# Kernel optimization log

Hardware: AMD Instinct MI355X
Metric: run time of the kernel (lower is better)

Reference implementation:

```python
import jax, jax.numpy as jnp
import numpy as np
from jax import lax

# Lens/aperture geometry (must match init_kwargs lens_mask)
LENS = 21
RADIUS = LENS // 2
EPS = 1e-8


def _offsets():
    """Flattened 21x21 aperture footprint: distance kernel, circular lens mask,
    and (row, col) slice offsets into the padded image."""
    ys, xs = np.meshgrid(np.arange(LENS), np.arange(LENS), indexing='ij')
    dy = ys - RADIUS
    dx = xs - RADIUS
    dist = np.sqrt(dy * dy + dx * dx).astype(np.float32)
    mask = (dist <= RADIUS).astype(np.float32)
    return (jnp.asarray(dist.ravel()), jnp.asarray(mask.ravel()),
            jnp.asarray(ys.ravel().astype(np.int32)),
            jnp.asarray(xs.ravel().astype(np.int32)))


def scatter_layer(x5, lens_effect):
    """Scatter (splat) defocus rendering of one RGBAD layer.

    x5: [B,5,H,W] (r,g,b,alpha,relative-disparity); lens_effect: [B,1].
    Each source pixel splats its premultiplied color over a disk of radius
    r = |disp| * lens_effect (soft-edged, area-normalized). Because the disk
    kernel is symmetric in the offset, the scatter is computed as a gather
    over the 21x21 footprint with weights taken from the *source* pixel.

    Returns [B,5,H,W]: [:3] accumulated rgb, [3] accumulated weight,
    [4] occupancy (clipped accumulated alpha-weight).
    """
    B, _, H, W = x5.shape
    dist, mask, oy, ox = _offsets()
    rgb, a, disp = x5[:, :3], x5[:, 3:4], x5[:, 4:5]
    r = jnp.clip(jnp.abs(disp) * lens_effect[:, :, None, None], 0.0, float(RADIUS))  # [B,1,H,W]

    # per-source-pixel soft disk area: sum_o mask(o) * clip(r + 0.5 - dist(o), 0, 1)
    def area_step(acc, dm):
        d, m = dm
        return acc + m * jnp.clip(r + 0.5 - d, 0.0, 1.0), None

    area, _ = lax.scan(area_step, jnp.zeros_like(r), (dist, mask))

    # premultiplied source energy, normalized by splat area
    s = jnp.concatenate([rgb * a, a], axis=1) / (area + EPS)  # [B,4,H,W]
    pad = ((0, 0), (0, 0), (RADIUS, RADIUS), (RADIUS, RADIUS))
    s_pad = jnp.pad(s, pad)
    r_pad = jnp.pad(r, pad)

    # gather formulation of the scatter: out[q] = sum_o s[q-o] * w(o; r[q-o])
    def step(acc, dmyx):
        d, m, dy, dx = dmyx
        sl = lax.dynamic_slice(s_pad, (0, 0, dy, dx), (B, 4, H, W))
        rsl = lax.dynamic_slice(r_pad, (0, 0, dy, dx), (B, 1, H, W))
        w = m * jnp.clip(rsl + 0.5 - d, 0.0, 1.0)
        return acc + sl * w, None

    out4, _ = lax.scan(step, jnp.zeros((B, 4, H, W), x5.dtype), (dist, mask, oy, ox))
    occu = jnp.clip(out4[:, 3:4], 0.0, 1.0)
    return jnp.concatenate([out4, occu], axis=1)


def setup_inputs() -> dict:
    key = jax.random.key(0)
    k1, k2 = jax.random.split(key)
    B, N_LAYER, H, W = 2, 3, 512, 512
    rgbad_layers = jax.random.uniform(k1, (B, 5 * N_LAYER, H, W), dtype=jnp.float32)
    # lens strength in a range that exercises the full 21x21 footprint
    lens_effect = jax.random.uniform(k2, (B, 1), dtype=jnp.float32) * 10.0
    focal = jnp.zeros((B, 5 * N_LAYER, H, W), dtype=jnp.float32)
    return {"rgbad_layers": rgbad_layers, "lens_effect": lens_effect, "focal": focal}


def reference(rgbad_layers, lens_effect, focal):
    """Multi_Layer_Renderer.forward: front-to-back alpha compositing of
    per-layer scatter-rendered bokeh."""
    x = rgbad_layers - focal
    n_layer = x.shape[1] // 5
    blurs = [scatter_layer(x[:, 5 * i:5 * (i + 1)], lens_effect) for i in range(n_layer)]
    rgb0, w0, o0 = blurs[0][:, :3], blurs[0][:, 3:4], blurs[0][:, 4:5]
    blur_rgb = rgb0 / (w0 + EPS) * o0
    trans = 1.0 - o0  # accumulated transmittance
    for li in range(1, n_layer):
        lr, lw, lo = blurs[li][:, :3], blurs[li][:, 3:4], blurs[li][:, 4:5]
        blur_rgb = blur_rgb + lr / (lw + EPS) * (trans * lo)
        trans = trans * (1.0 - lo)
    return blur_rgb
```

## Files before the change

### kernel.cpp

```cpp
#include <hip/hip_runtime.h>
#include <hip/hip_bf16.h>

#define HH 512
#define WW 512
#define HWSZ (512*512)

typedef _Float16 hh4 __attribute__((ext_vector_type(4)));

__device__ __forceinline__ float clamp01(float x) {
    return __builtin_amdgcn_fmed3f(x, 0.0f, 1.0f);
}

__global__ __launch_bounds__(256, 2)
void mlr_kernel(const float* __restrict__ rgbad,
                const float* __restrict__ lens_eff,
                const float* __restrict__ focal,
                float* __restrict__ out)
{
    constexpr int TW = 64, TH = 16;
    constexpr int SW = TW + 20;
    constexpr int SH = TH + 20;
    constexpr int LP = SW + 1;

    __shared__ uint2 sL[SH * LP];
    __shared__ float rL[SH * LP];
    __shared__ int   maxbits;

    const int tx  = threadIdx.x;
    const int ty  = threadIdx.y;
    const int tid = ty * 16 + tx;
    const int bx0 = blockIdx.x * TW;
    const int by0 = blockIdx.y * TH;
    const int bb  = blockIdx.z;
    const float lens = lens_eff[bb];

    static constexpr float DJ[44] = {
        0.f, 1.f, 1.41421356f, 2.f, 2.23606798f, 2.82842712f, 3.f, 3.16227766f,
        3.60555128f, 4.f, 4.12310563f, 4.24264069f, 4.47213595f, 5.f, 5.09901951f,
        5.38516481f, 5.65685425f, 5.83095189f, 6.f, 6.08276253f, 6.32455532f,
        6.40312424f, 6.70820393f, 7.f, 7.07106781f, 7.21110255f, 7.28010989f,
        7.61577311f, 7.81024968f, 8.f, 8.06225775f, 8.24621125f, 8.48528137f,
        8.54400375f, 8.60232527f, 8.94427191f, 9.f, 9.05538514f, 9.21954446f,
        9.43398113f, 9.48683298f, 9.84885780f, 9.89949494f, 10.f };
    static constexpr float CNT[44] = {
        1,4,4,4,8,4,4,8,8,4,8,4,8,12,8,8,4,8,4,8,8,8,
        8,4,12,8,8,8,8,4,16,8,4,8,8,8,4,8,16,8,8,8,4,12 };

    float blurR[4] = {0,0,0,0}, blurG[4] = {0,0,0,0}, blurB[4] = {0,0,0,0};
    float trans[4] = {1,1,1,1};

#pragma unroll 1
    for (int l = 0; l < 3; ++l) {
        __syncthreads();
        if (tid == 0) maxbits = 0;
        __syncthreads();

        const float* pin = rgbad + (size_t)(bb * 15 + 5 * l) * HWSZ;
        const float* pfo = focal + (size_t)(bb * 15 + 5 * l) * HWSZ;
        float mloc = 0.f;
#pragma unroll 1
        for (int i = tid; i < SH * SW; i += 256) {
            const int row = i / SW;
            const int col = i - row * SW;
            const int gy = by0 - 10 + row;
            const int gx = bx0 - 10 + col;
            uint2 pk; pk.x = 0u; pk.y = 0u;
            float rp05 = 0.f;
            if ((unsigned)gy < (unsigned)HH && (unsigned)gx < (unsigned)WW) {
                const int off = gy * WW + gx;
                const float cr = pin[off]            - pfo[off];
                const float cg = pin[off +   HWSZ]   - pfo[off +   HWSZ];
                const float cb = pin[off + 2*HWSZ]   - pfo[off + 2*HWSZ];
                const float ca = pin[off + 3*HWSZ]   - pfo[off + 3*HWSZ];
                const float cd = pin[off + 4*HWSZ]   - pfo[off + 4*HWSZ];
                const float r  = fminf(fabsf(cd) * lens, 10.f);
                rp05 = r + 0.5f;
                float a0 = 0.f, a1 = 0.f;
#pragma unroll
                for (int j = 0; j < 44; j += 2) {
                    a0 = fmaf(CNT[j],     clamp01(rp05 - DJ[j]),     a0);
                    a1 = fmaf(CNT[j + 1], clamp01(rp05 - DJ[j + 1]), a1);
                }
                const float inv = 1.0f / (a0 + a1 + 1e-8f);
                const float pa  = ca * inv;
                hh4 hv;
                hv.x = (_Float16)(cr * pa);
                hv.y = (_Float16)(cg * pa);
                hv.z = (_Float16)(cb * pa);
                hv.w = (_Float16)pa;
                pk = __builtin_bit_cast(uint2, hv);
                mloc = fmaxf(mloc, rp05);
            }
            sL[row * LP + col] = pk;
            rL[row * LP + col] = rp05;
        }
        atomicMax(&maxbits, __float_as_int(mloc));
        __syncthreads();

        const float rmax = __int_as_float(maxbits);
        const int U = min(10, (int)ceilf(rmax) - 1);

        float accR[4] = {0,0,0,0}, accG[4] = {0,0,0,0};
        float accB[4] = {0,0,0,0}, accW[4] = {0,0,0,0};

#pragma unroll 1
        for (int u = -U; u <= U; ++u) {
            const float u2f = (float)(u * u);
            float dd[21];
#pragma unroll
            for (int k = 0; k < 21; ++k) {
                const int dxk = k - 10;
                const float q = u2f + (float)(dxk * dxk);
                dd[k] = (q <= 100.0f) ? __builtin_sqrtf(q) : 1e9f;
            }
            const int rbase = (ty + 10 + u) * LP + 10 + 4 * tx;
#pragma unroll
            for (int v = -10; v <= 13; ++v) {
                const float rp = rL[rbase + v];
                const uint2 sp = sL[rbase + v];
                const hh4 hv = __builtin_bit_cast(hh4, sp);
                const float s0 = (float)hv.x;
                const float s1 = (float)hv.y;
                const float s2 = (float)hv.z;
                const float s3 = (float)hv.w;
#pragma unroll
                for (int ox = 0; ox < 4; ++ox) {
                    const int dx = v - ox;
                    if (dx >= -10 && dx <= 10) {
                        const float w = clamp01(rp - dd[dx + 10]);
                        accR[ox] = fmaf(s0, w, accR[ox]);
                        accG[ox] = fmaf(s1, w, accG[ox]);
                        accB[ox] = fmaf(s2, w, accB[ox]);
                        accW[ox] = fmaf(s3, w, accW[ox]);
                    }
                }
            }
        }

#pragma unroll
        for (int ox = 0; ox < 4; ++ox) {
            const float wsum = accW[ox];
            const float occ  = clamp01(wsum);
            const float f    = trans[ox] * occ / (wsum + 1e-8f);
            blurR[ox] = fmaf(accR[ox], f, blurR[ox]);
            blurG[ox] = fmaf(accG[ox], f, blurG[ox]);
            blurB[ox] = fmaf(accB[ox], f, blurB[ox]);
            trans[ox] *= (1.0f - occ);
        }
    }

    const int oy = by0 + ty;
    const size_t obase = (size_t)bb * 3 * HWSZ + (size_t)oy * WW + (size_t)(bx0 + 4 * tx);

    float4 vR, vG, vB;
    vR.x = blurR[0]; vR.y = blurR[1]; vR.z = blurR[2]; vR.w = blurR[3];
    vG.x = blurG[0]; vG.y = blurG[1]; vG.z = blurG[2]; vG.w = blurG[3];
    vB.x = blurB[0]; vB.y = blurB[1]; vB.z = blurB[2]; vB.w = blurB[3];

    *reinterpret_cast<float4*>(out + obase)            = vR;
    *reinterpret_cast<float4*>(out + obase + HWSZ)     = vG;
    *reinterpret_cast<float4*>(out + obase + 2 * HWSZ) = vB;
}

extern "C" void kernel_launch(void* const* d_in, const int* in_sizes, int n_in,
                              void* d_out, int out_size, void* d_ws, size_t ws_size,
                              hipStream_t stream) {
    const float* rgbad = (const float*)d_in[0];
    const float* lens  = (const float*)d_in[1];
    const float* focal = (const float*)d_in[2];
    float* out = (float*)d_out;
    const int B = in_sizes[1];
    dim3 grid(WW / 64, HH / 16, B);
    dim3 block(16, 16, 1);
    hipLaunchKernelGGL(mlr_kernel, grid, block, 0, stream, rgbad, lens, focal, out);
}
```

Before: 50.76 us.

## Split per-layer scatter into separate blocks and composite in second kernel

Launches one block per (batch, layer, tile) instead of looping layers within a block, tripling the grid to fill the GPU better and letting each layer tile use its own radius bound. Per-layer accumulators are stored in fp16 to a workspace and a second lightweight kernel performs the front-to-back compositing. This trades extra global memory traffic, a second launch and fp16 rounding of accumulated sums for higher parallelism. Falls back to the fused kernel when the workspace is too small.

Result: slower. 78.17 us (+54.0%).

```diff
diff --git a/kernel.cpp b/kernel.cpp
--- a/kernel.cpp
+++ b/kernel.cpp
@@ -11,16 +11,175 @@
     return __builtin_amdgcn_fmed3f(x, 0.0f, 1.0f);
 }
 
+__device__ __constant__ float DJ[44] = {
+    0.f, 1.f, 1.41421356f, 2.f, 2.23606798f, 2.82842712f, 3.f, 3.16227766f,
+    3.60555128f, 4.f, 4.12310563f, 4.24264069f, 4.47213595f, 5.f, 5.09901951f,
+    5.38516481f, 5.65685425f, 5.83095189f, 6.f, 6.08276253f, 6.32455532f,
+    6.40312424f, 6.70820393f, 7.f, 7.07106781f, 7.21110255f, 7.28010989f,
+    7.61577311f, 7.81024968f, 8.f, 8.06225775f, 8.24621125f, 8.48528137f,
+    8.54400375f, 8.60232527f, 8.94427191f, 9.f, 9.05538514f, 9.21954446f,
+    9.43398113f, 9.48683298f, 9.84885780f, 9.89949494f, 10.f };
+__device__ __constant__ float CNT[44] = {
+    1,4,4,4,8,4,4,8,8,4,8,4,8,12,8,8,4,8,4,8,8,8,
+    8,4,12,8,8,8,8,4,16,8,4,8,8,8,4,8,16,8,8,8,4,12 };
+
 __global__ __launch_bounds__(256, 2)
-void mlr_kernel(const float* __restrict__ rgbad,
-                const float* __restrict__ lens_eff,
-                const float* __restrict__ focal,
-                float* __restrict__ out)
+void mlr_layer_kernel(const float* __restrict__ rgbad,
+                      const float* __restrict__ lens_eff,
+                      const float* __restrict__ focal,
+                      uint2* __restrict__ ws)
 {
     constexpr int TW = 64, TH = 16;
     constexpr int SW = TW + 20;
     constexpr int SH = TH + 20;
     constexpr int LP = SW + 1;
+
+    __shared__ uint2 sL[SH * LP];
+    __shared__ float rL[SH * LP];
+    __shared__ int   maxbits;
+
+    const int tx  = threadIdx.x;
+    const int ty  = threadIdx.y;
+    const int tid = ty * 16 + tx;
+    const int bx0 = blockIdx.x * TW;
+    const int by0 = blockIdx.y * TH;
+    const int z   = blockIdx.z;
+    const int bb  = z / 3;
+    const float lens = lens_eff[bb];
+
+    if (tid == 0) maxbits = 0;
+    __syncthreads();
+
+    const float* pin = rgbad + (size_t)(bb * 15 + 5 * (z - bb * 3)) * HWSZ;
+    const float* pfo = focal + (size_t)(bb * 15 + 5 * (z - bb * 3)) * HWSZ;
+    float mloc = 0.f;
+#pragma unroll 1
+    for (int i = tid; i < SH * SW; i += 256) {
+        const int row = i / SW;
+        const int col = i - row * SW;
+        const int gy = by0 - 10 + row;
+        const int gx = bx0 - 10 + col;
+        uint2 pk; pk.x = 0u; pk.y = 0u;
+        float rp05 = 0.f;
+        if ((unsigned)gy < (unsigned)HH && (unsigned)gx < (unsigned)WW) {
+            const int off = gy * WW + gx;
+            const float cr = pin[off]            - pfo[off];
+            const float cg = pin[off +   HWSZ]   - pfo[off +   HWSZ];
+            const float cb = pin[off + 2*HWSZ]   - pfo[off + 2*HWSZ];
+            const float ca = pin[off + 3*HWSZ]   - pfo[off + 3*HWSZ];
+            const float cd = pin[off + 4*HWSZ]   - pfo[off + 4*HWSZ];
+            const float r  = fminf(fabsf(cd) * lens, 10.f);
+            rp05 = r + 0.5f;
+            float a0 = 0.f, a1 = 0.f;
+#pragma unroll
+            for (int j = 0; j < 44; j += 2) {
+                a0 = fmaf(CNT[j],     clamp01(rp05 - DJ[j]),     a0);
+                a1 = fmaf(CNT[j + 1], clamp01(rp05 - DJ[j + 1]), a1);
+            }
+            const float inv = 1.0f / (a0 + a1 + 1e-8f);
+            const float pa  = ca * inv;
+            hh4 hv;
+            hv.x = (_Float16)(cr * pa);
+            hv.y = (_Float16)(cg * pa);
+            hv.z = (_Float16)(cb * pa);
+            hv.w = (_Float16)pa;
+            pk = __builtin_bit_cast(uint2, hv);
+            mloc = fmaxf(mloc, rp05);
+        }
+        sL[row * LP + col] = pk;
+        rL[row * LP + col] = rp05;
+    }
+    atomicMax(&maxbits, __float_as_int(mloc));
+    __syncthreads();
+
+    const float rmax = __int_as_float(maxbits);
+    const int U = min(10, (int)ceilf(rmax) - 1);
+
+    float accR[4] = {0,0,0,0}, accG[4] = {0,0,0,0};
+    float accB[4] = {0,0,0,0}, accW[4] = {0,0,0,0};
+
+#pragma unroll 1
+    for (int u = -U; u <= U; ++u) {
+        const float u2f = (float)(u * u);
+        float dd[21];
+#pragma unroll
+        for (int k = 0; k < 21; ++k) {
+            const int dxk = k - 10;
+            const float q = u2f + (float)(dxk * dxk);
+            dd[k] = (q <= 100.0f) ? __builtin_sqrtf(q) : 1e9f;
+        }
+        const int rbase = (ty + 10 + u) * LP + 10 + 4 * tx;
+#pragma unroll
+        for (int v = -10; v <= 13; ++v) {
+            const float rp = rL[rbase + v];
+            const uint2 sp = sL[rbase + v];
+            const hh4 hv = __builtin_bit_cast(hh4, sp);
+            const float s0 = (float)hv.x;
+            const float s1 = (float)hv.y;
+            const float s2 = (float)hv.z;
+            const float s3 = (float)hv.w;
+#pragma unroll
+            for (int ox = 0; ox < 4; ++ox) {
+                const int dx = v - ox;
+                if (dx >= -10 && dx <= 10) {
+                    const float w = clamp01(rp - dd[dx + 10]);
+                    accR[ox] = fmaf(s0, w, accR[ox]);
+                    accG[ox] = fmaf(s1, w, accG[ox]);
+                    accB[ox] = fmaf(s2, w, accB[ox]);
+                    accW[ox] = fmaf(s3, w, accW[ox]);
+                }
+            }
+        }
+    }
+
+    auto pk1 = [&](int ox) -> uint2 {
+        hh4 h;
+        h.x = (_Float16)accR[ox]; h.y = (_Float16)accG[ox];
+        h.z = (_Float16)accB[ox]; h.w = (_Float16)accW[ox];
+        return __builtin_bit_cast(uint2, h);
+    };
+    uint4 w01, w23;
+    { uint2 a = pk1(0), b = pk1(1); w01.x = a.x; w01.y = a.y; w01.z = b.x; w01.w = b.y; }
+    { uint2 a = pk1(2), b = pk1(3); w23.x = a.x; w23.y = a.y; w23.z = b.x; w23.w = b.y; }
+
+    const size_t wbase = (size_t)z * HWSZ + (size_t)(by0 + ty) * WW + (size_t)(bx0 + 4 * tx);
+    *reinterpret_cast<uint4*>(ws + wbase)     = w01;
+    *reinterpret_cast<uint4*>(ws + wbase + 2) = w23;
+}
+
+__global__ __launch_bounds__(256, 4)
+void mlr_comp_kernel(const uint2* __restrict__ ws, float* __restrict__ out)
+{
+    const int p = blockIdx.x * 256 + threadIdx.x;
+    const int b = p >> 18;
+    const int i = p & (HWSZ - 1);
+
+    float blurR = 0.f, blurG = 0.f, blurB = 0.f, trans = 1.f;
+#pragma unroll
+    for (int l = 0; l < 3; ++l) {
+        const uint2 v = ws[(size_t)(b * 3 + l) * HWSZ + i];
+        const hh4 h = __builtin_bit_cast(hh4, v);
+        const float wsum = (float)h.w;
+        const float occ  = clamp01(wsum);
+        const float f    = trans * occ / (wsum + 1e-8f);
+        blurR = fmaf((float)h.x, f, blurR);
+        blurG = fmaf((float)h.y, f, blurG);
+        blurB = fmaf((float)h.z, f, blurB);
+        trans *= (1.0f - occ);
+    }
+    out[(size_t)(b * 3 + 0) * HWSZ + i] = blurR;
+    out[(size_t)(b * 3 + 1) * HWSZ + i] = blurG;
+    out[(size_t)(b * 3 + 2) * HWSZ + i] = blurB;
+}
+
+__global__ __launch_bounds__(256, 2)
+void mlr_fused_kernel(const float* __restrict__ rgbad,
+                      const float* __restrict__ lens_eff,
+                      const float* __restrict__ focal,
+                      float* __restrict__ out)
+{
+    constexpr int TW = 64, TH = 16;
+    constexpr int SW = TW + 20, SH = TH + 20, LP = SW + 1;
 
     __shared__ uint2 sL[SH * LP];
     __shared__ float rL[SH * LP];
@@ -33,18 +192,6 @@
     const int by0 = blockIdx.y * TH;
     const int bb  = blockIdx.z;
     const float lens = lens_eff[bb];
-
-    static constexpr float DJ[44] = {
-        0.f, 1.f, 1.41421356f, 2.f, 2.23606798f, 2.82842712f, 3.f, 3.16227766f,
-        3.60555128f, 4.f, 4.12310563f, 4.24264069f, 4.47213595f, 5.f, 5.09901951f,
-        5.38516481f, 5.65685425f, 5.83095189f, 6.f, 6.08276253f, 6.32455532f,
-        6.40312424f, 6.70820393f, 7.f, 7.07106781f, 7.21110255f, 7.28010989f,
-        7.61577311f, 7.81024968f, 8.f, 8.06225775f, 8.24621125f, 8.48528137f,
-        8.54400375f, 8.60232527f, 8.94427191f, 9.f, 9.05538514f, 9.21954446f,
-        9.43398113f, 9.48683298f, 9.84885780f, 9.89949494f, 10.f };
-    static constexpr float CNT[44] = {
-        1,4,4,4,8,4,4,8,8,4,8,4,8,12,8,8,4,8,4,8,8,8,
-        8,4,12,8,8,8,8,4,16,8,4,8,8,8,4,8,16,8,8,8,4,12 };
 
     float blurR[4] = {0,0,0,0}, blurG[4] = {0,0,0,0}, blurB[4] = {0,0,0,0};
     float trans[4] = {1,1,1,1};
@@ -170,7 +317,21 @@
     const float* focal = (const float*)d_in[2];
     float* out = (float*)d_out;
     const int B = in_sizes[1];
-    dim3 grid(WW / 64, HH / 16, B);
-    dim3 block(16, 16, 1);
-    hipLaunchKernelGGL(mlr_kernel, grid, block, 0, stream, rgbad, lens, focal, out);
-}
+
+    const size_t ws_need = (size_t)B * 3 * HWSZ * sizeof(uint2);
+    if (ws_size >= ws_need) {
+        dim3 grid1(WW / 64, HH / 16, 3 * B);
+        dim3 block1(16, 16, 1);
+        hipLaunchKernelGGL(mlr_layer_kernel, grid1, block1, 0, stream,
+                           rgbad, lens, focal, (uint2*)d_ws);
+        dim3 grid2((B * HWSZ) / 256, 1, 1);
+        dim3 block2(256, 1, 1);
+        hipLaunchKernelGGL(mlr_comp_kernel, grid2, block2, 0, stream,
+                           (const uint2*)d_ws, out);
+    } else {
+        dim3 grid(WW / 64, HH / 16, B);
+        dim3 block(16, 16, 1);
+        hipLaunchKernelGGL(mlr_fused_kernel, grid, block, 0, stream,
+                           rgbad, lens, focal, out);
+    }
+}
```

## Skip out-of-disk horizontal taps per row, vectorize tile loads, raise occupancy

Applied to the files above, without the earlier changes.

The gather loop over each aperture row now always runs a central band of horizontal taps. The outer bands of taps run only when the tile's maximum radius, given the row offset, can reach them, so the summed work follows a disk instead of a square. The shared tile is widened to 88 columns so staging can use aligned float4 loads of input and focal data, with four pixels per thread slot. Launch bounds move from 2 to 4 blocks per CU, which caps registers per thread and risks spills in the heavily unrolled tap code.

Result: faster. 45.83 us (-9.7%).

```diff
diff --git a/kernel.cpp b/kernel.cpp
--- a/kernel.cpp
+++ b/kernel.cpp
@@ -6,21 +6,24 @@
 #define HWSZ (512*512)
 
 typedef _Float16 hh4 __attribute__((ext_vector_type(4)));
+typedef float    ff4 __attribute__((ext_vector_type(4)));
 
 __device__ __forceinline__ float clamp01(float x) {
     return __builtin_amdgcn_fmed3f(x, 0.0f, 1.0f);
 }
 
-__global__ __launch_bounds__(256, 2)
-void mlr_kernel(const float* __restrict__ rgbad,
-                const float* __restrict__ lens_eff,
-                const float* __restrict__ focal,
-                float* __restrict__ out)
+__global__ __launch_bounds__(256, 4)
+void mlr_fused_kernel(const float* __restrict__ rgbad,
+                      const float* __restrict__ lens_eff,
+                      const float* __restrict__ focal,
+                      float* __restrict__ out)
 {
     constexpr int TW = 64, TH = 16;
-    constexpr int SW = TW + 20;
+    constexpr int SW = 88;
     constexpr int SH = TH + 20;
     constexpr int LP = SW + 1;
+    constexpr int NG = SW / 4;
+    constexpr int NSLOT = SH * NG;
 
     __shared__ uint2 sL[SH * LP];
     __shared__ float rL[SH * LP];
@@ -58,23 +61,40 @@
         const float* pin = rgbad + (size_t)(bb * 15 + 5 * l) * HWSZ;
         const float* pfo = focal + (size_t)(bb * 15 + 5 * l) * HWSZ;
         float mloc = 0.f;
+
 #pragma unroll 1
-        for (int i = tid; i < SH * SW; i += 256) {
-            const int row = i / SW;
-            const int col = i - row * SW;
-            const int gy = by0 - 10 + row;
-            const int gx = bx0 - 10 + col;
-            uint2 pk; pk.x = 0u; pk.y = 0u;
-            float rp05 = 0.f;
-            if ((unsigned)gy < (unsigned)HH && (unsigned)gx < (unsigned)WW) {
-                const int off = gy * WW + gx;
-                const float cr = pin[off]            - pfo[off];
-                const float cg = pin[off +   HWSZ]   - pfo[off +   HWSZ];
-                const float cb = pin[off + 2*HWSZ]   - pfo[off + 2*HWSZ];
-                const float ca = pin[off + 3*HWSZ]   - pfo[off + 3*HWSZ];
-                const float cd = pin[off + 4*HWSZ]   - pfo[off + 4*HWSZ];
+        for (int s = tid; s < NSLOT; s += 256) {
+            const int row = s / NG;
+            const int grp = s - row * NG;
+            const int gy  = by0 - 10 + row;
+            const int gx0 = bx0 - 12 + 4 * grp;
+
+            ff4 i0 = {0,0,0,0}, i1 = {0,0,0,0}, i2 = {0,0,0,0}, i3 = {0,0,0,0}, i4 = {0,0,0,0};
+            ff4 f0 = {0,0,0,0}, f1 = {0,0,0,0}, f2 = {0,0,0,0}, f3 = {0,0,0,0}, f4 = {0,0,0,0};
+            const bool valid = ((unsigned)gy < (unsigned)HH) && ((unsigned)gx0 < (unsigned)WW);
+            if (valid) {
+                const size_t off = (size_t)gy * WW + (size_t)gx0;
+                i0 = *reinterpret_cast<const ff4*>(pin + off);
+                i1 = *reinterpret_cast<const ff4*>(pin + off +   HWSZ);
+                i2 = *reinterpret_cast<const ff4*>(pin + off + 2*HWSZ);
+                i3 = *reinterpret_cast<const ff4*>(pin + off + 3*HWSZ);
+                i4 = *reinterpret_cast<const ff4*>(pin + off + 4*HWSZ);
+                f0 = *reinterpret_cast<const ff4*>(pfo + off);
+                f1 = *reinterpret_cast<const ff4*>(pfo + off +   HWSZ);
+                f2 = *reinterpret_cast<const ff4*>(pfo + off + 2*HWSZ);
+                f3 = *reinterpret_cast<const ff4*>(pfo + off + 3*HWSZ);
+                f4 = *reinterpret_cast<const ff4*>(pfo + off + 4*HWSZ);
+            }
+            const int base = row * LP + 4 * grp;
+#pragma unroll
+            for (int k = 0; k < 4; ++k) {
+                const float cr = i0[k] - f0[k];
+                const float cg = i1[k] - f1[k];
+                const float cb = i2[k] - f2[k];
+                const float ca = i3[k] - f3[k];
+                const float cd = i4[k] - f4[k];
                 const float r  = fminf(fabsf(cd) * lens, 10.f);
-                rp05 = r + 0.5f;
+                const float rp05 = r + 0.5f;
                 float a0 = 0.f, a1 = 0.f;
 #pragma unroll
                 for (int j = 0; j < 44; j += 2) {
@@ -88,11 +108,13 @@
                 hv.y = (_Float16)(cg * pa);
                 hv.z = (_Float16)(cb * pa);
                 hv.w = (_Float16)pa;
-                pk = __builtin_bit_cast(uint2, hv);
-                mloc = fmaxf(mloc, rp05);
-            }
-            sL[row * LP + col] = pk;
-            rL[row * LP + col] = rp05;
+                sL[base + k] = __builtin_bit_cast(uint2, hv);
+                rL[base + k] = rp05;
+            }
+            if (valid) mloc = fmaxf(mloc, fminf(fabsf(i4[0]-f4[0])*lens,10.f)+0.5f);
+            if (valid) mloc = fmaxf(mloc, fminf(fabsf(i4[1]-f4[1])*lens,10.f)+0.5f);
+            if (valid) mloc = fmaxf(mloc, fminf(fabsf(i4[2]-f4[2])*lens,10.f)+0.5f);
+            if (valid) mloc = fmaxf(mloc, fminf(fabsf(i4[3]-f4[3])*lens,10.f)+0.5f);
         }
         atomicMax(&maxbits, __float_as_int(mloc));
         __syncthreads();
@@ -103,9 +125,25 @@
         float accR[4] = {0,0,0,0}, accG[4] = {0,0,0,0};
         float accB[4] = {0,0,0,0}, accW[4] = {0,0,0,0};
 
+#define TAP(vv) { \
+            const float rp = rL[rbase + (vv)]; \
+            const hh4 hv = __builtin_bit_cast(hh4, sL[rbase + (vv)]); \
+            const float s0 = (float)hv.x, s1 = (float)hv.y; \
+            const float s2 = (float)hv.z, s3 = (float)hv.w; \
+            _Pragma("unroll") \
+            for (int ox = 0; ox < 4; ++ox) { \
+                const int dx = (vv) - ox; \
+                if (dx >= -10 && dx <= 10) { \
+                    const float w = clamp01(rp - dd[dx + 10]); \
+                    accR[ox] = fmaf(s0, w, accR[ox]); \
+                    accG[ox] = fmaf(s1, w, accG[ox]); \
+                    accB[ox] = fmaf(s2, w, accB[ox]); \
+                    accW[ox] = fmaf(s3, w, accW[ox]); } } }
+
 #pragma unroll 1
         for (int u = -U; u <= U; ++u) {
             const float u2f = (float)(u * u);
+            const float vm2 = rmax * rmax - u2f;
             float dd[21];
 #pragma unroll
             for (int k = 0; k < 21; ++k) {
@@ -113,29 +151,30 @@
                 const float q = u2f + (float)(dxk * dxk);
                 dd[k] = (q <= 100.0f) ? __builtin_sqrtf(q) : 1e9f;
             }
-            const int rbase = (ty + 10 + u) * LP + 10 + 4 * tx;
-#pragma unroll
-            for (int v = -10; v <= 13; ++v) {
-                const float rp = rL[rbase + v];
-                const uint2 sp = sL[rbase + v];
-                const hh4 hv = __builtin_bit_cast(hh4, sp);
-                const float s0 = (float)hv.x;
-                const float s1 = (float)hv.y;
-                const float s2 = (float)hv.z;
-                const float s3 = (float)hv.w;
-#pragma unroll
-                for (int ox = 0; ox < 4; ++ox) {
-                    const int dx = v - ox;
-                    if (dx >= -10 && dx <= 10) {
-                        const float w = clamp01(rp - dd[dx + 10]);
-                        accR[ox] = fmaf(s0, w, accR[ox]);
-                        accG[ox] = fmaf(s1, w, accG[ox]);
-                        accB[ox] = fmaf(s2, w, accB[ox]);
-                        accW[ox] = fmaf(s3, w, accW[ox]);
-                    }
-                }
+            const int rbase = (ty + 10 + u) * LP + 12 + 4 * tx;
+
+#pragma unroll
+            for (int v = -2; v <= 5; ++v) TAP(v);
+            if (vm2 > 9.0f) {
+#pragma unroll
+                for (int v = -5; v <= -3; ++v) TAP(v);
+#pragma unroll
+                for (int v = 6; v <= 8; ++v) TAP(v);
+            }
+            if (vm2 > 36.0f) {
+#pragma unroll
+                for (int v = -8; v <= -6; ++v) TAP(v);
+#pragma unroll
+                for (int v = 9; v <= 11; ++v) TAP(v);
+            }
+            if (vm2 > 81.0f) {
+#pragma unroll
+                for (int v = -10; v <= -9; ++v) TAP(v);
+#pragma unroll
+                for (int v = 12; v <= 13; ++v) TAP(v);
             }
         }
+#undef TAP
 
 #pragma unroll
         for (int ox = 0; ox < 4; ++ox) {
@@ -172,5 +211,6 @@
     const int B = in_sizes[1];
     dim3 grid(WW / 64, HH / 16, B);
     dim3 block(16, 16, 1);
-    hipLaunchKernelGGL(mlr_kernel, grid, block, 0, stream, rgbad, lens, focal, out);
+    hipLaunchKernelGGL(mlr_fused_kernel, grid, block, 0, stream,
+                       rgbad, lens, focal, out);
 }
```
